# Kernel tuning notes

Hardware: AMD Instinct MI355X
Metric: run time of the kernel (lower is better)

Reference implementation:

```python
import jax, jax.numpy as jnp
import numpy as np

B, T, I, R, H = 8, 2048, 128, 1024, 256
LEAKY = 1.0           # leaky_rate
SPECTRAL_RADIUS = 0.9


def setup_inputs() -> dict:
    key = jax.random.key(0)
    ks = jax.random.split(key, 8)
    u = jax.random.normal(ks[0], (B, T, I), dtype=jnp.float32)
    # ESN cell weights (fixed random reservoir)
    w_in = jax.random.normal(ks[1], (R, I), dtype=jnp.float32) * (1.0 / np.sqrt(I))  # input_scaling=1
    w = jax.random.normal(ks[2], (R, R), dtype=jnp.float32) * (SPECTRAL_RADIUS / np.sqrt(R))
    w_bias = jnp.zeros((R,), dtype=jnp.float32)  # bias_scaling=0
    # PCA stand-in: fixed linear projection reservoir -> pca space
    w_pca = jax.random.normal(ks[3], (R, H), dtype=jnp.float32) * (1.0 / np.sqrt(R))
    # gate weights: torch.rand -> uniform [0,1)
    wzp = jax.random.uniform(ks[4], (H, H), dtype=jnp.float32)
    wzh = jax.random.uniform(ks[5], (H, H), dtype=jnp.float32)
    bz = jax.random.uniform(ks[6], (H,), dtype=jnp.float32)
    return {"u": u, "w_in": w_in, "w": w, "w_bias": w_bias,
            "w_pca": w_pca, "wzp": wzp, "wzh": wzh, "bz": bz}


def reference(u, w_in, w, w_bias, w_pca, wzp, wzh, bz):
    Bn = u.shape[0]
    Rd = w.shape[0]
    Hd = bz.shape[0]
    # Precompute input drive for all timesteps: (T, B, R)
    uin = jnp.swapaxes(jnp.einsum('bti,ri->btr', u, w_in) + w_bias, 0, 1)

    # ESN leaky reservoir recurrence: x_t = (1-a)x_{t-1} + a*tanh(W_in u_t + W x_{t-1} + b)
    def res_step(x, u_t):
        x_new = (1.0 - LEAKY) * x + LEAKY * jnp.tanh(u_t + x @ w.T)
        return x_new, x_new

    x0 = jnp.zeros((Bn, Rd), dtype=u.dtype)
    _, res_states = jax.lax.scan(res_step, x0, uin)          # (T, B, R)

    # PCA projection (linear stand-in for fitted IncrementalPCA)
    pca_states = jnp.einsum('tbr,rh->tbh', res_states, w_pca)  # (T, B, H)

    # Gated recurrence: z_t = sigmoid(Wzp p_t + Wzh h_{t-1} + bz); h_t = (1-z)*h + z*p
    def gate_step(h, p):
        z = jax.nn.sigmoid(p @ wzp.T + h @ wzh.T + bz)
        h_new = (1.0 - z) * h + z * p
        return h_new, h_new

    h0 = jnp.zeros((Bn, Hd), dtype=u.dtype)  # per-batch reset_hidden()
    _, hidden_states = jax.lax.scan(gate_step, h0, pca_states)  # (T, B, H)
    return jnp.swapaxes(hidden_states, 0, 1)                    # (B, T, H)
```

## Files before the change

### kernel.cpp

```cpp
#include <hip/hip_runtime.h>
#include <hip/hip_bf16.h>

#define TSTEPS 2048
#define NCHAIN 8
#define RDIM 1024
#define IDIM 128
#define HDIM 256
#define NB 16
#define NTHR 512
#define NBLOCKS (NB * NCHAIN)

typedef unsigned long long u64_t;

#define PIN(x) asm volatile("" : "+v"(x))

__device__ __forceinline__ float aload(const float* p) {
  return __hip_atomic_load(p, __ATOMIC_RELAXED, __HIP_MEMORY_SCOPE_AGENT);
}
__device__ __forceinline__ void astore(float* p, float v) {
  __hip_atomic_store(p, v, __ATOMIC_RELAXED, __HIP_MEMORY_SCOPE_AGENT);
}
__device__ __forceinline__ float2 aload2(const float* p) {
  u64_t q = __hip_atomic_load(reinterpret_cast<const u64_t*>(p),
                              __ATOMIC_RELAXED, __HIP_MEMORY_SCOPE_AGENT);
  union { u64_t u; float2 f; } c; c.u = q;
  return c.f;
}

__device__ __forceinline__ float wave_sum(float v) {
  v += __shfl_xor(v, 1);
  v += __shfl_xor(v, 2);
  v += __shfl_xor(v, 4);
  v += __shfl_xor(v, 8);
  v += __shfl_xor(v, 16);
  v += __shfl_xor(v, 32);
  return v;
}

__device__ __forceinline__ void gbar(unsigned* cnt, unsigned target) {
  asm volatile("s_waitcnt vmcnt(0) lgkmcnt(0)" ::: "memory");
  __syncthreads();
  if (threadIdx.x == 0) {
    __hip_atomic_fetch_add(cnt, 1u, __ATOMIC_RELAXED, __HIP_MEMORY_SCOPE_AGENT);
    unsigned it = 0;
    while (__hip_atomic_load(cnt, __ATOMIC_RELAXED, __HIP_MEMORY_SCOPE_AGENT) < target) {
      __builtin_amdgcn_s_sleep(1);
      if (++it > (1u << 15)) break;
    }
  }
  __syncthreads();
}

__global__ __launch_bounds__(NTHR, 1) void esn_fused(
    const float* __restrict__ u, const float* __restrict__ w_in,
    const float* __restrict__ w, const float* __restrict__ w_bias,
    const float* __restrict__ w_pca, const float* __restrict__ wzp,
    const float* __restrict__ wzh, const float* __restrict__ bz,
    float* __restrict__ out,
    float* __restrict__ x_buf,
    float* __restrict__ p_buf,
    float* __restrict__ h_buf,
    unsigned* __restrict__ barr)
{
  const int bid = blockIdx.x;
  const int chain = bid & 7;
  const int sub = bid >> 3;
  const int tid = threadIdx.x;
  const int wave = tid >> 6;
  const int lane = tid & 63;
  unsigned* cnt = barr + chain * 64;

  const int rrow0 = sub * 64 + wave * 8;
  float4 WA[8][4];
  #pragma unroll
  for (int j = 0; j < 8; ++j)
    #pragma unroll
    for (int i = 0; i < 4; ++i)
      WA[j][i] = *reinterpret_cast<const float4*>(
          w + (size_t)(rrow0 + j) * RDIM + lane * 16 + i * 4);
  float2 Wi[8];
  #pragma unroll
  for (int j = 0; j < 8; ++j)
    Wi[j] = *reinterpret_cast<const float2*>(w_in + (size_t)(rrow0 + j) * IDIM + lane * 2);
  float wb = (lane < 8) ? w_bias[rrow0 + lane] : 0.f;

  const int pcol0 = sub * 16 + wave * 2;
  float Wp[2][16];
  #pragma unroll
  for (int j = 0; j < 2; ++j)
    #pragma unroll
    for (int k = 0; k < 16; ++k)
      Wp[j][k] = w_pca[(size_t)(lane * 16 + k) * HDIM + pcol0 + j];

  const int grow0 = sub * 16 + wave * 2;
  float4 Zp[2], Zh[2];
  #pragma unroll
  for (int j = 0; j < 2; ++j) {
    Zp[j] = *reinterpret_cast<const float4*>(wzp + (size_t)(grow0 + j) * HDIM + lane * 4);
    Zh[j] = *reinterpret_cast<const float4*>(wzh + (size_t)(grow0 + j) * HDIM + lane * 4);
  }
  float bzr = (lane < 2) ? bz[grow0 + lane] : 0.f;

  #pragma unroll
  for (int j = 0; j < 8; ++j)
    #pragma unroll
    for (int i = 0; i < 4; ++i) {
      PIN(WA[j][i].x); PIN(WA[j][i].y); PIN(WA[j][i].z); PIN(WA[j][i].w);
    }
  #pragma unroll
  for (int j = 0; j < 8; ++j) { PIN(Wi[j].x); PIN(Wi[j].y); }
  #pragma unroll
  for (int j = 0; j < 2; ++j)
    #pragma unroll
    for (int k = 0; k < 16; ++k) PIN(Wp[j][k]);
  #pragma unroll
  for (int j = 0; j < 2; ++j) {
    PIN(Zp[j].x); PIN(Zp[j].y); PIN(Zp[j].z); PIN(Zp[j].w);
    PIN(Zh[j].x); PIN(Zh[j].y); PIN(Zh[j].z); PIN(Zh[j].w);
  }
  PIN(wb); PIN(bzr);

  for (int s = 0; s < TSTEPS + 2; ++s) {
    float xc[16];
    const bool xc_valid = (s >= 1 && s <= TSTEPS);
    if (xc_valid) {
      const float* xp = x_buf + ((((s - 1) & 1) * NCHAIN) + chain) * RDIM + lane * 16;
      #pragma unroll
      for (int k = 0; k < 8; ++k) {
        float2 f = aload2(xp + 2 * k);
        xc[2 * k] = f.x;
        xc[2 * k + 1] = f.y;
      }
    }

    if (s < TSTEPS) {
      float acc[8];
      float2 uu = *reinterpret_cast<const float2*>(
          u + ((size_t)chain * TSTEPS + s) * IDIM + lane * 2);
      #pragma unroll
      for (int j = 0; j < 8; ++j) acc[j] = Wi[j].x * uu.x + Wi[j].y * uu.y;
      if (s > 0) {
        #pragma unroll
        for (int j = 0; j < 8; ++j) {
          float a = acc[j];
          #pragma unroll
          for (int i = 0; i < 4; ++i) {
            a += WA[j][i].x * xc[i * 4 + 0];
            a += WA[j][i].y * xc[i * 4 + 1];
            a += WA[j][i].z * xc[i * 4 + 2];
            a += WA[j][i].w * xc[i * 4 + 3];
          }
          acc[j] = a;
        }
      }
      #pragma unroll
      for (int j = 0; j < 8; ++j) acc[j] = wave_sum(acc[j]);
      float v = acc[0];
      #pragma unroll
      for (int j = 1; j < 8; ++j) v = (lane == j) ? acc[j] : v;
      if (lane < 8)
        astore(x_buf + (((s & 1) * NCHAIN) + chain) * RDIM + rrow0 + lane,
               tanhf(v + wb));
    }

    if (xc_valid) {
      const int t = s - 1;
      float a0 = 0.f, a1 = 0.f;
      #pragma unroll
      for (int k = 0; k < 16; ++k) { a0 += Wp[0][k] * xc[k]; a1 += Wp[1][k] * xc[k]; }
      a0 = wave_sum(a0);
      a1 = wave_sum(a1);
      float v = (lane == 1) ? a1 : a0;
      if (lane < 2)
        astore(p_buf + (((t & 1) * NCHAIN) + chain) * HDIM + pcol0 + lane, v);
    }

    if (s >= 2) {
      const int t = s - 2;
      const float* pv = p_buf + (((t & 1) * NCHAIN) + chain) * HDIM;
      const float* hv = h_buf + ((((t - 1) & 1) * NCHAIN) + chain) * HDIM;
      float pc[4], hc[4];
      {
        float2 f0 = aload2(pv + lane * 4), f1 = aload2(pv + lane * 4 + 2);
        pc[0] = f0.x; pc[1] = f0.y; pc[2] = f1.x; pc[3] = f1.y;
      }
      if (t > 0) {
        float2 f0 = aload2(hv + lane * 4), f1 = aload2(hv + lane * 4 + 2);
        hc[0] = f0.x; hc[1] = f0.y; hc[2] = f1.x; hc[3] = f1.y;
      } else {
        hc[0] = hc[1] = hc[2] = hc[3] = 0.f;
      }
      float a0 = Zp[0].x * pc[0] + Zp[0].y * pc[1] + Zp[0].z * pc[2] + Zp[0].w * pc[3]
               + Zh[0].x * hc[0] + Zh[0].y * hc[1] + Zh[0].z * hc[2] + Zh[0].w * hc[3];
      float a1 = Zp[1].x * pc[0] + Zp[1].y * pc[1] + Zp[1].z * pc[2] + Zp[1].w * pc[3]
               + Zh[1].x * hc[0] + Zh[1].y * hc[1] + Zh[1].z * hc[2] + Zh[1].w * hc[3];
      a0 = wave_sum(a0);
      a1 = wave_sum(a1);
      float v = (lane == 1) ? a1 : a0;
      if (lane < 2) {
        const int row = grow0 + lane;
        float z = 1.f / (1.f + expf(-(v + bzr)));
        float pt = aload(pv + row);
        float hp = (t > 0) ? aload(hv + row) : 0.f;
        float hnew = hp + z * (pt - hp);
        astore(h_buf + (((t & 1) * NCHAIN) + chain) * HDIM + row, hnew);
        out[((size_t)chain * TSTEPS + t) * HDIM + row] = hnew;
      }
    }

    if (s <= TSTEPS) gbar(cnt, (unsigned)(s + 1) * NB);
  }
}

extern "C" void kernel_launch(void* const* d_in, const int* in_sizes, int n_in,
                              void* d_out, int out_size, void* d_ws, size_t ws_size,
                              hipStream_t stream) {
  const float* ptrs[8] = {nullptr};
  const int want[8] = {TSTEPS * NCHAIN * IDIM, RDIM * IDIM, RDIM * RDIM, RDIM,
                       RDIM * HDIM, HDIM * HDIM, HDIM * HDIM, HDIM};
  if (n_in == 8) {
    int used[8] = {0};
    for (int k = 0; k < 8; ++k)
      for (int i = 0; i < n_in; ++i)
        if (!used[i] && in_sizes[i] == want[k]) {
          ptrs[k] = (const float*)d_in[i]; used[i] = 1; break;
        }
  }
  bool ok = true;
  for (int k = 0; k < 8; ++k) ok = ok && (ptrs[k] != nullptr);
  if (!ok)
    for (int k = 0; k < 8; ++k) ptrs[k] = (const float*)d_in[k];

  float* out = (float*)d_out;

  float* x_buf = (float*)d_ws;
  float* p_buf = x_buf + 2 * NCHAIN * RDIM;
  float* h_buf = p_buf + 2 * NCHAIN * HDIM;
  unsigned* barr = (unsigned*)(h_buf + 2 * NCHAIN * HDIM);
  size_t zero_floats =
      (size_t)(2 * NCHAIN * RDIM + 2 * NCHAIN * HDIM * 2 + NCHAIN * 64);
  if (ws_size < zero_floats * 4) return;
  hipMemsetAsync(d_ws, 0, zero_floats * 4, stream);

  esn_fused<<<dim3(NBLOCKS), dim3(NTHR), 0, stream>>>(
      ptrs[0], ptrs[1], ptrs[2], ptrs[3], ptrs[4], ptrs[5], ptrs[6], ptrs[7],
      out, x_buf, p_buf, h_buf, barr);
}
```

Measured before the change: 10.99 ms.

## Replace per-step global barrier with tagged-value dataflow synchronization

Removes the per-chain atomic-counter barrier that ran after every timestep. Each value written to the reservoir, PCA and hidden-state exchange buffers is now a 64-bit word holding the float plus a step tag, and consumers spin on the tags of exactly the data they need. The p and h buffers grow from two slots to four so a fast block cannot overwrite data a slower block still has to read. The goal is to cut barrier latency and let blocks proceed as soon as their inputs arrive, at the cost of doubled exchange traffic, per-lane polling, and dropping the workspace memset in favour of tag matching.

```diff
diff --git a/kernel.cpp b/kernel.cpp
--- a/kernel.cpp
+++ b/kernel.cpp
@@ -1,5 +1,4 @@
 #include <hip/hip_runtime.h>
-#include <hip/hip_bf16.h>
 
 #define TSTEPS 2048
 #define NCHAIN 8
@@ -14,18 +13,17 @@
 
 #define PIN(x) asm volatile("" : "+v"(x))
 
-__device__ __forceinline__ float aload(const float* p) {
+__device__ __forceinline__ u64_t aload64(const u64_t* p) {
   return __hip_atomic_load(p, __ATOMIC_RELAXED, __HIP_MEMORY_SCOPE_AGENT);
 }
-__device__ __forceinline__ void astore(float* p, float v) {
+__device__ __forceinline__ void astore64(u64_t* p, u64_t v) {
   __hip_atomic_store(p, v, __ATOMIC_RELAXED, __HIP_MEMORY_SCOPE_AGENT);
 }
-__device__ __forceinline__ float2 aload2(const float* p) {
-  u64_t q = __hip_atomic_load(reinterpret_cast<const u64_t*>(p),
-                              __ATOMIC_RELAXED, __HIP_MEMORY_SCOPE_AGENT);
-  union { u64_t u; float2 f; } c; c.u = q;
-  return c.f;
-}
+__device__ __forceinline__ u64_t pack(float v, unsigned tag) {
+  return ((u64_t)tag << 32) | (u64_t)__float_as_uint(v);
+}
+__device__ __forceinline__ float val_of(u64_t q) { return __uint_as_float((unsigned)q); }
+__device__ __forceinline__ unsigned tag_of(u64_t q) { return (unsigned)(q >> 32); }
 
 __device__ __forceinline__ float wave_sum(float v) {
   v += __shfl_xor(v, 1);
@@ -37,30 +35,15 @@
   return v;
 }
 
-__device__ __forceinline__ void gbar(unsigned* cnt, unsigned target) {
-  asm volatile("s_waitcnt vmcnt(0) lgkmcnt(0)" ::: "memory");
-  __syncthreads();
-  if (threadIdx.x == 0) {
-    __hip_atomic_fetch_add(cnt, 1u, __ATOMIC_RELAXED, __HIP_MEMORY_SCOPE_AGENT);
-    unsigned it = 0;
-    while (__hip_atomic_load(cnt, __ATOMIC_RELAXED, __HIP_MEMORY_SCOPE_AGENT) < target) {
-      __builtin_amdgcn_s_sleep(1);
-      if (++it > (1u << 15)) break;
-    }
-  }
-  __syncthreads();
-}
-
 __global__ __launch_bounds__(NTHR, 1) void esn_fused(
     const float* __restrict__ u, const float* __restrict__ w_in,
     const float* __restrict__ w, const float* __restrict__ w_bias,
     const float* __restrict__ w_pca, const float* __restrict__ wzp,
     const float* __restrict__ wzh, const float* __restrict__ bz,
     float* __restrict__ out,
-    float* __restrict__ x_buf,
-    float* __restrict__ p_buf,
-    float* __restrict__ h_buf,
-    unsigned* __restrict__ barr)
+    u64_t* __restrict__ x_buf,
+    u64_t* __restrict__ p_buf,
+    u64_t* __restrict__ h_buf)
 {
   const int bid = blockIdx.x;
   const int chain = bid & 7;
@@ -68,7 +51,6 @@
   const int tid = threadIdx.x;
   const int wave = tid >> 6;
   const int lane = tid & 63;
-  unsigned* cnt = barr + chain * 64;
 
   const int rrow0 = sub * 64 + wave * 8;
   float4 WA[8][4];
@@ -124,13 +106,23 @@
     float xc[16];
     const bool xc_valid = (s >= 1 && s <= TSTEPS);
     if (xc_valid) {
-      const float* xp = x_buf + ((((s - 1) & 1) * NCHAIN) + chain) * RDIM + lane * 16;
-      #pragma unroll
-      for (int k = 0; k < 8; ++k) {
-        float2 f = aload2(xp + 2 * k);
-        xc[2 * k] = f.x;
-        xc[2 * k + 1] = f.y;
-      }
+      const u64_t* xp =
+          x_buf + ((((s - 1) & 1) * NCHAIN) + chain) * RDIM + lane * 16;
+      const unsigned want = (unsigned)s;
+      u64_t q[16];
+      unsigned it = 0;
+      for (;;) {
+        bool ok = true;
+        #pragma unroll
+        for (int k = 0; k < 16; ++k) q[k] = aload64(xp + k);
+        #pragma unroll
+        for (int k = 0; k < 16; ++k) ok = ok & (tag_of(q[k]) == want);
+        if (ok) break;
+        __builtin_amdgcn_s_sleep(1);
+        if (++it > (1u << 15)) break;
+      }
+      #pragma unroll
+      for (int k = 0; k < 16; ++k) xc[k] = val_of(q[k]);
     }
 
     if (s < TSTEPS) {
@@ -159,8 +151,8 @@
       #pragma unroll
       for (int j = 1; j < 8; ++j) v = (lane == j) ? acc[j] : v;
       if (lane < 8)
-        astore(x_buf + (((s & 1) * NCHAIN) + chain) * RDIM + rrow0 + lane,
-               tanhf(v + wb));
+        astore64(x_buf + (((s & 1) * NCHAIN) + chain) * RDIM + rrow0 + lane,
+                 pack(tanhf(v + wb), (unsigned)(s + 1)));
     }
 
     if (xc_valid) {
@@ -172,23 +164,51 @@
       a1 = wave_sum(a1);
       float v = (lane == 1) ? a1 : a0;
       if (lane < 2)
-        astore(p_buf + (((t & 1) * NCHAIN) + chain) * HDIM + pcol0 + lane, v);
+        astore64(p_buf + (((t & 3) * NCHAIN) + chain) * HDIM + pcol0 + lane,
+                 pack(v, (unsigned)(t + 1)));
     }
 
     if (s >= 2) {
       const int t = s - 2;
-      const float* pv = p_buf + (((t & 1) * NCHAIN) + chain) * HDIM;
-      const float* hv = h_buf + ((((t - 1) & 1) * NCHAIN) + chain) * HDIM;
+      const u64_t* pv = p_buf + (((t & 3) * NCHAIN) + chain) * HDIM;
+      const u64_t* hv = h_buf + ((((t - 1) & 3) * NCHAIN) + chain) * HDIM;
       float pc[4], hc[4];
-      {
-        float2 f0 = aload2(pv + lane * 4), f1 = aload2(pv + lane * 4 + 2);
-        pc[0] = f0.x; pc[1] = f0.y; pc[2] = f1.x; pc[3] = f1.y;
-      }
+      const unsigned wantp = (unsigned)(t + 1);
+      const unsigned wanth = (unsigned)t;
       if (t > 0) {
-        float2 f0 = aload2(hv + lane * 4), f1 = aload2(hv + lane * 4 + 2);
-        hc[0] = f0.x; hc[1] = f0.y; hc[2] = f1.x; hc[3] = f1.y;
+        u64_t qp[4], qh[4];
+        unsigned it = 0;
+        for (;;) {
+          bool ok = true;
+          #pragma unroll
+          for (int k = 0; k < 4; ++k) {
+            qp[k] = aload64(pv + lane * 4 + k);
+            qh[k] = aload64(hv + lane * 4 + k);
+          }
+          #pragma unroll
+          for (int k = 0; k < 4; ++k)
+            ok = ok & (tag_of(qp[k]) == wantp) & (tag_of(qh[k]) == wanth);
+          if (ok) break;
+          __builtin_amdgcn_s_sleep(1);
+          if (++it > (1u << 15)) break;
+        }
+        #pragma unroll
+        for (int k = 0; k < 4; ++k) { pc[k] = val_of(qp[k]); hc[k] = val_of(qh[k]); }
       } else {
-        hc[0] = hc[1] = hc[2] = hc[3] = 0.f;
+        u64_t qp[4];
+        unsigned it = 0;
+        for (;;) {
+          bool ok = true;
+          #pragma unroll
+          for (int k = 0; k < 4; ++k) qp[k] = aload64(pv + lane * 4 + k);
+          #pragma unroll
+          for (int k = 0; k < 4; ++k) ok = ok & (tag_of(qp[k]) == wantp);
+          if (ok) break;
+          __builtin_amdgcn_s_sleep(1);
+          if (++it > (1u << 15)) break;
+        }
+        #pragma unroll
+        for (int k = 0; k < 4; ++k) { pc[k] = val_of(qp[k]); hc[k] = 0.f; }
       }
       float a0 = Zp[0].x * pc[0] + Zp[0].y * pc[1] + Zp[0].z * pc[2] + Zp[0].w * pc[3]
                + Zh[0].x * hc[0] + Zh[0].y * hc[1] + Zh[0].z * hc[2] + Zh[0].w * hc[3];
@@ -200,15 +220,14 @@
       if (lane < 2) {
         const int row = grow0 + lane;
         float z = 1.f / (1.f + expf(-(v + bzr)));
-        float pt = aload(pv + row);
-        float hp = (t > 0) ? aload(hv + row) : 0.f;
+        float pt = val_of(aload64(pv + row));
+        float hp = (t > 0) ? val_of(aload64(hv + row)) : 0.f;
         float hnew = hp + z * (pt - hp);
-        astore(h_buf + (((t & 1) * NCHAIN) + chain) * HDIM + row, hnew);
+        astore64(h_buf + (((t & 3) * NCHAIN) + chain) * HDIM + row,
+                 pack(hnew, (unsigned)(t + 1)));
         out[((size_t)chain * TSTEPS + t) * HDIM + row] = hnew;
       }
     }
-
-    if (s <= TSTEPS) gbar(cnt, (unsigned)(s + 1) * NB);
   }
 }
 
@@ -233,16 +252,13 @@
 
   float* out = (float*)d_out;
 
-  float* x_buf = (float*)d_ws;
-  float* p_buf = x_buf + 2 * NCHAIN * RDIM;
-  float* h_buf = p_buf + 2 * NCHAIN * HDIM;
-  unsigned* barr = (unsigned*)(h_buf + 2 * NCHAIN * HDIM);
-  size_t zero_floats =
-      (size_t)(2 * NCHAIN * RDIM + 2 * NCHAIN * HDIM * 2 + NCHAIN * 64);
-  if (ws_size < zero_floats * 4) return;
-  hipMemsetAsync(d_ws, 0, zero_floats * 4, stream);
+  u64_t* x_buf = (u64_t*)d_ws;
+  u64_t* p_buf = x_buf + 2 * NCHAIN * RDIM;
+  u64_t* h_buf = p_buf + 4 * NCHAIN * HDIM;
+  size_t need_u64 = (size_t)(2 * NCHAIN * RDIM + 2 * 4 * NCHAIN * HDIM);
+  if (ws_size < need_u64 * 8) return;
 
   esn_fused<<<dim3(NBLOCKS), dim3(NTHR), 0, stream>>>(
       ptrs[0], ptrs[1], ptrs[2], ptrs[3], ptrs[4], ptrs[5], ptrs[6], ptrs[7],
-      out, x_buf, p_buf, h_buf, barr);
-}
+      out, x_buf, p_buf, h_buf);
+}
```

Result: slower. 24.42 ms (+122.1%).
